# Optimization experiments

Measured on AMD Instinct MI355X. Metric: run time of the kernel, lower is better.

The kernel has to match this reference:

```python
import jax, jax.numpy as jnp
import numpy as np

N = 100000   # nodes
E = 1600000  # edges
C = 128      # in_channels
H = 128      # hidden_channels


def _gcn_conv(x, row, col, w, W, b, n_nodes):
    """PyG-style GCNConv: x' = D^{-1/2}(A+I)D^{-1/2} (x W) + b, with edge weights."""
    x = x @ W  # [N, out]
    # add self-loops with weight 1
    loop = jnp.arange(n_nodes, dtype=row.dtype)
    row2 = jnp.concatenate([row, loop])
    col2 = jnp.concatenate([col, loop])
    w2 = jnp.concatenate([w, jnp.ones((n_nodes,), dtype=w.dtype)])
    # symmetric normalization: deg over destination (col), per PyG gcn_norm
    deg = jax.ops.segment_sum(w2, col2, num_segments=n_nodes)
    dinv = jnp.where(deg > 0, jax.lax.rsqrt(jnp.where(deg > 0, deg, 1.0)), 0.0)
    norm = dinv[row2] * w2 * dinv[col2]  # [E+N]
    # message = norm * x[src]; aggregate (scatter-add) into dst
    msg = norm[:, None] * x[row2]  # [E+N, out]
    out = jax.ops.segment_sum(msg, col2, num_segments=n_nodes)
    return out + b


def setup_inputs() -> dict:
    key = jax.random.key(0)
    k0, k1, k2, k3, k4 = jax.random.split(key, 5)
    node_feature = jax.random.normal(k0, (N, C), dtype=jnp.float32)
    edge_index = jax.random.randint(k1, (2, E), 0, N, dtype=jnp.int32)
    edge_weight = jax.random.uniform(k2, (E,), dtype=jnp.float32)
    W1 = jax.random.normal(k3, (C, H), dtype=jnp.float32) * (1.0 / np.sqrt(C))
    b1 = jnp.zeros((H,), dtype=jnp.float32)
    W2 = jax.random.normal(k4, (H, 1), dtype=jnp.float32) * (1.0 / np.sqrt(H))
    b2 = jnp.zeros((1,), dtype=jnp.float32)
    return {"node_feature": node_feature, "edge_index": edge_index,
            "edge_weight": edge_weight, "W1": W1, "b1": b1, "W2": W2, "b2": b2}


def reference(node_feature, edge_index, edge_weight, W1, b1, W2, b2):
    row, col = edge_index[0], edge_index[1]
    h = _gcn_conv(node_feature, row, col, edge_weight, W1, b1, N)
    out = _gcn_conv(h, row, col, edge_weight, W2, b2, N)  # [N, 1]
    return out
```

## Files before the change

### kernel.cpp

```cpp
#include <hip/hip_runtime.h>

#define CH 128
#define CHUNK 8192
#define BSH 9
#define BNODES 512
#define MAXB 256

__global__ __launch_bounds__(256) void k_uw(const float* __restrict__ W1,
                                            const float* __restrict__ b1,
                                            const float* __restrict__ W2,
                                            float* __restrict__ u) {
    int wid  = blockIdx.x * 4 + (threadIdx.x >> 6);
    if (wid > CH) return;
    int lane = threadIdx.x & 63;
    const float* rowp = (wid < CH) ? (W1 + (size_t)wid * CH) : b1;
    float2 xv = *(const float2*)(rowp + lane * 2);
    float2 vv = *(const float2*)(W2 + lane * 2);
    float acc = xv.x * vv.x + xv.y * vv.y;
#pragma unroll
    for (int m = 32; m; m >>= 1) acc += __shfl_xor(acc, m);
    if (lane == 0) u[wid] = acc;
}

__global__ __launch_bounds__(256) void k_gemv(const float* __restrict__ X,
                                              const float* __restrict__ v,
                                              float* __restrict__ t, int n) {
    int wv   = blockIdx.x * 4 + (threadIdx.x >> 6);
    int lane = threadIdx.x & 63;
    int row  = wv * 2 + (lane >> 5);
    if (row >= n) return;
    float4 xv = *(const float4*)(X + (size_t)row * CH + (lane & 31) * 4);
    float4 vv = *(const float4*)(v + (lane & 31) * 4);
    float acc = xv.x * vv.x + xv.y * vv.y + xv.z * vv.z + xv.w * vv.w;
#pragma unroll
    for (int m = 16; m; m >>= 1) acc += __shfl_xor(acc, m);
    if ((lane & 31) == 0) t[row] = acc;
}

__global__ __launch_bounds__(256) void k_hist(const int* __restrict__ col,
                                              int* __restrict__ Ht,
                                              int nbuck, int e_cnt) {
    __shared__ int h[MAXB];
    int b = blockIdx.x, tid = threadIdx.x;
    if (tid < nbuck) h[tid] = 0;
    __syncthreads();
    int e0 = b * CHUNK, e1 = min(e0 + CHUNK, e_cnt);
    for (int e = e0 + tid; e < e1; e += 256)
        atomicAdd(&h[col[e] >> BSH], 1);
    __syncthreads();
    if (tid < nbuck) Ht[(size_t)b * nbuck + tid] = h[tid];
}

__global__ __launch_bounds__(256) void k_colscan(const int* __restrict__ Ht,
                                                 int* __restrict__ Hs,
                                                 int* __restrict__ coltot,
                                                 int nchunk, int nbuck) {
    int j = blockIdx.x * 4 + (threadIdx.x >> 6);
    if (j >= nbuck) return;
    int lane = threadIdx.x & 63;
    int run = 0;
    for (int base = 0; base < nchunk; base += 64) {
        int idx = base + lane;
        int v = (idx < nchunk) ? Ht[(size_t)idx * nbuck + j] : 0;
        int incl = v;
#pragma unroll
        for (int d = 1; d < 64; d <<= 1) {
            int up = __shfl_up(incl, d);
            if (lane >= d) incl += up;
        }
        if (idx < nchunk) Hs[(size_t)idx * nbuck + j] = run + incl - v;
        run += __shfl(incl, 63);
    }
    if (lane == 0) coltot[j] = run;
}

__global__ __launch_bounds__(256) void k_permute(const int* __restrict__ row,
                                                 const int* __restrict__ col,
                                                 const float* __restrict__ w,
                                                 const int* __restrict__ Hs,
                                                 const int* __restrict__ coltot,
                                                 int* __restrict__ bstart,
                                                 int2* __restrict__ ep,
                                                 int nbuck, int e_cnt) {
    __shared__ int ct[MAXB];
    __shared__ int bs[MAXB + 1];
    __shared__ int cur[MAXB];
    int b = blockIdx.x, tid = threadIdx.x;
    for (int k = tid; k < nbuck; k += 256) ct[k] = coltot[k];
    __syncthreads();
    if (tid < 64) {
        int vals[4]; int sum = 0;
#pragma unroll
        for (int k = 0; k < 4; ++k) {
            int idx = tid * 4 + k;
            vals[k] = (idx < nbuck) ? ct[idx] : 0;
            sum += vals[k];
        }
        int incl = sum;
#pragma unroll
        for (int d = 1; d < 64; d <<= 1) {
            int up = __shfl_up(incl, d);
            if (tid >= d) incl += up;
        }
        int run = incl - sum;
#pragma unroll
        for (int k = 0; k < 4; ++k) {
            int idx = tid * 4 + k;
            if (idx < nbuck) bs[idx] = run;
            run += vals[k];
        }
        if (tid == 63) bs[nbuck] = run;
    }
    __syncthreads();
    for (int k = tid; k < nbuck; k += 256) cur[k] = bs[k] + Hs[(size_t)b * nbuck + k];
    __syncthreads();
    int e0 = b * CHUNK, e1 = min(e0 + CHUNK, e_cnt);
    for (int e = e0 + tid; e < e1; e += 256) {
        int r = row[e], c = col[e];
        float wv = w[e];
        int pos = atomicAdd(&cur[c >> BSH], 1);
        ep[pos] = make_int2(r | ((c & (BNODES - 1)) << 17), __float_as_int(wv));
    }
    if (b == 0)
        for (int k = tid; k <= nbuck; k += 256) bstart[k] = bs[k];
}

__global__ __launch_bounds__(512) void k_adeg(const int2* __restrict__ ep,
                                              const int* __restrict__ bstart,
                                              const float* __restrict__ t,
                                              float* __restrict__ dinv,
                                              float* __restrict__ p, int n) {
    __shared__ float acc[BNODES];
    int b = blockIdx.x, tid = threadIdx.x;
    acc[tid] = 0.f;
    __syncthreads();
    int j1 = bstart[b + 1];
    for (int j = bstart[b] + tid; j < j1; j += 512) {
        int2 kv = ep[j];
        atomicAdd(&acc[kv.x >> 17], __int_as_float(kv.y));
    }
    __syncthreads();
    int node = (b << BSH) + tid;
    if (node < n) {
        float di = rsqrtf(1.0f + acc[tid]);
        dinv[node] = di;
        p[node] = di * t[node];
    }
}

__global__ __launch_bounds__(512) void k_as1(const int2* __restrict__ ep,
                                             const int* __restrict__ bstart,
                                             const float* __restrict__ p,
                                             const float* __restrict__ dinv,
                                             const float* __restrict__ u,
                                             float* __restrict__ q, int n) {
    __shared__ float acc[BNODES];
    int b = blockIdx.x, tid = threadIdx.x;
    acc[tid] = 0.f;
    __syncthreads();
    int j1 = bstart[b + 1];
    for (int j = bstart[b] + tid; j < j1; j += 512) {
        int2 kv = ep[j];
        atomicAdd(&acc[kv.x >> 17], __int_as_float(kv.y) * p[kv.x & 0x1FFFF]);
    }
    __syncthreads();
    int node = (b << BSH) + tid;
    if (node < n) {
        float di = dinv[node];
        float s1 = di * (p[node] + acc[tid]);
        q[node] = di * (s1 + u[CH]);
    }
}

__global__ __launch_bounds__(512) void k_aout(const int2* __restrict__ ep,
                                              const int* __restrict__ bstart,
                                              const float* __restrict__ q,
                                              const float* __restrict__ dinv,
                                              const float* __restrict__ b2,
                                              float* __restrict__ out, int n) {
    __shared__ float acc[BNODES];
    int b = blockIdx.x, tid = threadIdx.x;
    acc[tid] = 0.f;
    __syncthreads();
    int j1 = bstart[b + 1];
    for (int j = bstart[b] + tid; j < j1; j += 512) {
        int2 kv = ep[j];
        atomicAdd(&acc[kv.x >> 17], __int_as_float(kv.y) * q[kv.x & 0x1FFFF]);
    }
    __syncthreads();
    int node = (b << BSH) + tid;
    if (node < n)
        out[node] = b2[0] + dinv[node] * (q[node] + acc[tid]);
}

extern "C" void kernel_launch(void* const* d_in, const int* in_sizes, int n_in,
                              void* d_out, int out_size, void* d_ws, size_t ws_size,
                              hipStream_t stream) {
    const float* x   = (const float*)d_in[0];
    const int*   ei  = (const int*)d_in[1];
    const float* w   = (const float*)d_in[2];
    const float* W1  = (const float*)d_in[3];
    const float* b1  = (const float*)d_in[4];
    const float* W2  = (const float*)d_in[5];
    const float* b2  = (const float*)d_in[6];
    float* out = (float*)d_out;

    const int n     = in_sizes[0] / CH;
    const int e_cnt = in_sizes[2];
    const int* row = ei;
    const int* col = ei + e_cnt;

    const int nbuck  = (n + BNODES - 1) >> BSH;
    const int nchunk = (e_cnt + CHUNK - 1) / CHUNK;

    int2*  ep     = (int2*)d_ws;
    float* u      = (float*)(ep + e_cnt);
    float* t      = u + 132;
    float* dinv   = t + n;
    float* p      = dinv + n;
    float* q      = p + n;
    int*   coltot = (int*)(q + n);
    int*   bstart = coltot + nbuck;
    int*   Ht     = bstart + nbuck + 1;
    int*   Hs     = Ht + (size_t)nchunk * nbuck;

    k_uw<<<(CH + 1 + 3) / 4, 256, 0, stream>>>(W1, b1, W2, u);
    k_gemv<<<(n + 7) / 8, 256, 0, stream>>>(x, u, t, n);

    k_hist<<<nchunk, 256, 0, stream>>>(col, Ht, nbuck, e_cnt);
    k_colscan<<<(nbuck + 3) / 4, 256, 0, stream>>>(Ht, Hs, coltot, nchunk, nbuck);
    k_permute<<<nchunk, 256, 0, stream>>>(row, col, w, Hs, coltot, bstart, ep, nbuck, e_cnt);

    k_adeg<<<nbuck, 512, 0, stream>>>(ep, bstart, t, dinv, p, n);
    k_as1<<<nbuck, 512, 0, stream>>>(ep, bstart, p, dinv, u, q, n);
    k_aout<<<nbuck, 512, 0, stream>>>(ep, bstart, q, dinv, b2, out, n);
}
```

Measured before the change: 174.3 us.

## Fuse sort and aggregation stages into one persistent kernel with grid barriers

Replaces the six separate histogram, scan, permute and three aggregation kernels with a single kernel that synchronises stages through a software grid barrier built on global atomics. The column scan is folded into each block, which re-reads the histogram table. The GEMV is also turned into a grid-stride loop over four rows per iteration with a fixed grid. The aim is to remove launch overhead and the gaps between dependent kernels. In exchange it relies on all blocks (about 196) being co-resident to avoid deadlock, and adds a redundant O(nchunk) scan per block plus barrier spin cost.

```diff
diff --git a/kernel.cpp b/kernel.cpp
--- a/kernel.cpp
+++ b/kernel.cpp
@@ -5,11 +5,32 @@
 #define BSH 9
 #define BNODES 512
 #define MAXB 256
+#define NT 512
+
+__device__ __forceinline__ void gsync(int* bar, int nb, int it) {
+    __syncthreads();
+    if (threadIdx.x == 0) {
+        __threadfence();
+        if (__hip_atomic_fetch_add(&bar[0], 1, __ATOMIC_ACQ_REL,
+                                   __HIP_MEMORY_SCOPE_AGENT) == nb - 1) {
+            __hip_atomic_store(&bar[0], 0, __ATOMIC_RELAXED, __HIP_MEMORY_SCOPE_AGENT);
+            __hip_atomic_fetch_add(&bar[1], 1, __ATOMIC_RELEASE, __HIP_MEMORY_SCOPE_AGENT);
+        } else {
+            while (__hip_atomic_load(&bar[1], __ATOMIC_ACQUIRE,
+                                     __HIP_MEMORY_SCOPE_AGENT) < it)
+                __builtin_amdgcn_s_sleep(8);
+        }
+        __threadfence();
+    }
+    __syncthreads();
+}
 
 __global__ __launch_bounds__(256) void k_uw(const float* __restrict__ W1,
                                             const float* __restrict__ b1,
                                             const float* __restrict__ W2,
-                                            float* __restrict__ u) {
+                                            float* __restrict__ u,
+                                            int* __restrict__ bar) {
+    if (blockIdx.x == 0 && threadIdx.x == 0) { bar[0] = 0; bar[1] = 0; }
     int wid  = blockIdx.x * 4 + (threadIdx.x >> 6);
     if (wid > CH) return;
     int lane = threadIdx.x & 63;
@@ -23,174 +44,172 @@
 }
 
 __global__ __launch_bounds__(256) void k_gemv(const float* __restrict__ X,
-                                              const float* __restrict__ v,
+                                              const float* __restrict__ u,
                                               float* __restrict__ t, int n) {
-    int wv   = blockIdx.x * 4 + (threadIdx.x >> 6);
-    int lane = threadIdx.x & 63;
-    int row  = wv * 2 + (lane >> 5);
-    if (row >= n) return;
-    float4 xv = *(const float4*)(X + (size_t)row * CH + (lane & 31) * 4);
-    float4 vv = *(const float4*)(v + (lane & 31) * 4);
-    float acc = xv.x * vv.x + xv.y * vv.y + xv.z * vv.z + xv.w * vv.w;
-#pragma unroll
-    for (int m = 16; m; m >>= 1) acc += __shfl_xor(acc, m);
-    if ((lane & 31) == 0) t[row] = acc;
-}
-
-__global__ __launch_bounds__(256) void k_hist(const int* __restrict__ col,
-                                              int* __restrict__ Ht,
-                                              int nbuck, int e_cnt) {
-    __shared__ int h[MAXB];
-    int b = blockIdx.x, tid = threadIdx.x;
-    if (tid < nbuck) h[tid] = 0;
-    __syncthreads();
-    int e0 = b * CHUNK, e1 = min(e0 + CHUNK, e_cnt);
-    for (int e = e0 + tid; e < e1; e += 256)
-        atomicAdd(&h[col[e] >> BSH], 1);
-    __syncthreads();
-    if (tid < nbuck) Ht[(size_t)b * nbuck + tid] = h[tid];
-}
-
-__global__ __launch_bounds__(256) void k_colscan(const int* __restrict__ Ht,
-                                                 int* __restrict__ Hs,
-                                                 int* __restrict__ coltot,
-                                                 int nchunk, int nbuck) {
-    int j = blockIdx.x * 4 + (threadIdx.x >> 6);
-    if (j >= nbuck) return;
-    int lane = threadIdx.x & 63;
-    int run = 0;
-    for (int base = 0; base < nchunk; base += 64) {
-        int idx = base + lane;
-        int v = (idx < nchunk) ? Ht[(size_t)idx * nbuck + j] : 0;
-        int incl = v;
-#pragma unroll
-        for (int d = 1; d < 64; d <<= 1) {
-            int up = __shfl_up(incl, d);
-            if (lane >= d) incl += up;
-        }
-        if (idx < nchunk) Hs[(size_t)idx * nbuck + j] = run + incl - v;
-        run += __shfl(incl, 63);
-    }
-    if (lane == 0) coltot[j] = run;
-}
-
-__global__ __launch_bounds__(256) void k_permute(const int* __restrict__ row,
-                                                 const int* __restrict__ col,
-                                                 const float* __restrict__ w,
-                                                 const int* __restrict__ Hs,
-                                                 const int* __restrict__ coltot,
-                                                 int* __restrict__ bstart,
-                                                 int2* __restrict__ ep,
-                                                 int nbuck, int e_cnt) {
-    __shared__ int ct[MAXB];
-    __shared__ int bs[MAXB + 1];
-    __shared__ int cur[MAXB];
-    int b = blockIdx.x, tid = threadIdx.x;
-    for (int k = tid; k < nbuck; k += 256) ct[k] = coltot[k];
-    __syncthreads();
-    if (tid < 64) {
-        int vals[4]; int sum = 0;
-#pragma unroll
-        for (int k = 0; k < 4; ++k) {
-            int idx = tid * 4 + k;
-            vals[k] = (idx < nbuck) ? ct[idx] : 0;
-            sum += vals[k];
-        }
-        int incl = sum;
-#pragma unroll
-        for (int d = 1; d < 64; d <<= 1) {
-            int up = __shfl_up(incl, d);
-            if (tid >= d) incl += up;
-        }
-        int run = incl - sum;
-#pragma unroll
-        for (int k = 0; k < 4; ++k) {
-            int idx = tid * 4 + k;
-            if (idx < nbuck) bs[idx] = run;
-            run += vals[k];
-        }
-        if (tid == 63) bs[nbuck] = run;
-    }
-    __syncthreads();
-    for (int k = tid; k < nbuck; k += 256) cur[k] = bs[k] + Hs[(size_t)b * nbuck + k];
-    __syncthreads();
-    int e0 = b * CHUNK, e1 = min(e0 + CHUNK, e_cnt);
-    for (int e = e0 + tid; e < e1; e += 256) {
-        int r = row[e], c = col[e];
-        float wv = w[e];
-        int pos = atomicAdd(&cur[c >> BSH], 1);
-        ep[pos] = make_int2(r | ((c & (BNODES - 1)) << 17), __float_as_int(wv));
-    }
-    if (b == 0)
-        for (int k = tid; k <= nbuck; k += 256) bstart[k] = bs[k];
-}
-
-__global__ __launch_bounds__(512) void k_adeg(const int2* __restrict__ ep,
-                                              const int* __restrict__ bstart,
-                                              const float* __restrict__ t,
-                                              float* __restrict__ dinv,
-                                              float* __restrict__ p, int n) {
-    __shared__ float acc[BNODES];
-    int b = blockIdx.x, tid = threadIdx.x;
-    acc[tid] = 0.f;
-    __syncthreads();
-    int j1 = bstart[b + 1];
-    for (int j = bstart[b] + tid; j < j1; j += 512) {
-        int2 kv = ep[j];
-        atomicAdd(&acc[kv.x >> 17], __int_as_float(kv.y));
-    }
-    __syncthreads();
-    int node = (b << BSH) + tid;
-    if (node < n) {
-        float di = rsqrtf(1.0f + acc[tid]);
-        dinv[node] = di;
-        p[node] = di * t[node];
-    }
-}
-
-__global__ __launch_bounds__(512) void k_as1(const int2* __restrict__ ep,
-                                             const int* __restrict__ bstart,
-                                             const float* __restrict__ p,
-                                             const float* __restrict__ dinv,
+    int hw = blockIdx.x * 8 + (threadIdx.x >> 5);
+    int l  = threadIdx.x & 31;
+    float4 uv = *(const float4*)(u + l * 4);
+    const int stride = gridDim.x * 8;
+    for (int base = hw; base < n; base += stride * 4) {
+        int r0 = base, r1 = base + stride, r2 = base + 2 * stride, r3 = base + 3 * stride;
+        float a0 = 0.f, a1 = 0.f, a2 = 0.f, a3 = 0.f;
+        if (r0 < n) { float4 x = *(const float4*)(X + (size_t)r0 * CH + l * 4);
+                      a0 = x.x * uv.x + x.y * uv.y + x.z * uv.z + x.w * uv.w; }
+        if (r1 < n) { float4 x = *(const float4*)(X + (size_t)r1 * CH + l * 4);
+                      a1 = x.x * uv.x + x.y * uv.y + x.z * uv.z + x.w * uv.w; }
+        if (r2 < n) { float4 x = *(const float4*)(X + (size_t)r2 * CH + l * 4);
+                      a2 = x.x * uv.x + x.y * uv.y + x.z * uv.z + x.w * uv.w; }
+        if (r3 < n) { float4 x = *(const float4*)(X + (size_t)r3 * CH + l * 4);
+                      a3 = x.x * uv.x + x.y * uv.y + x.z * uv.z + x.w * uv.w; }
+#pragma unroll
+        for (int m = 16; m; m >>= 1) {
+            a0 += __shfl_xor(a0, m); a1 += __shfl_xor(a1, m);
+            a2 += __shfl_xor(a2, m); a3 += __shfl_xor(a3, m);
+        }
+        if (l == 0) {
+            if (r0 < n) t[r0] = a0;
+            if (r1 < n) t[r1] = a1;
+            if (r2 < n) t[r2] = a2;
+            if (r3 < n) t[r3] = a3;
+        }
+    }
+}
+
+__global__ __launch_bounds__(NT) void k_mega(const int* __restrict__ row,
+                                             const int* __restrict__ col,
+                                             const float* __restrict__ w,
+                                             const float* __restrict__ t,
                                              const float* __restrict__ u,
-                                             float* __restrict__ q, int n) {
-    __shared__ float acc[BNODES];
-    int b = blockIdx.x, tid = threadIdx.x;
-    acc[tid] = 0.f;
-    __syncthreads();
-    int j1 = bstart[b + 1];
-    for (int j = bstart[b] + tid; j < j1; j += 512) {
-        int2 kv = ep[j];
-        atomicAdd(&acc[kv.x >> 17], __int_as_float(kv.y) * p[kv.x & 0x1FFFF]);
-    }
-    __syncthreads();
-    int node = (b << BSH) + tid;
-    if (node < n) {
-        float di = dinv[node];
-        float s1 = di * (p[node] + acc[tid]);
-        q[node] = di * (s1 + u[CH]);
-    }
-}
-
-__global__ __launch_bounds__(512) void k_aout(const int2* __restrict__ ep,
-                                              const int* __restrict__ bstart,
-                                              const float* __restrict__ q,
-                                              const float* __restrict__ dinv,
-                                              const float* __restrict__ b2,
-                                              float* __restrict__ out, int n) {
-    __shared__ float acc[BNODES];
-    int b = blockIdx.x, tid = threadIdx.x;
-    acc[tid] = 0.f;
-    __syncthreads();
-    int j1 = bstart[b + 1];
-    for (int j = bstart[b] + tid; j < j1; j += 512) {
-        int2 kv = ep[j];
-        atomicAdd(&acc[kv.x >> 17], __int_as_float(kv.y) * q[kv.x & 0x1FFFF]);
-    }
-    __syncthreads();
-    int node = (b << BSH) + tid;
-    if (node < n)
-        out[node] = b2[0] + dinv[node] * (q[node] + acc[tid]);
+                                             const float* __restrict__ b2,
+                                             int2* __restrict__ ep,
+                                             int* __restrict__ Ht,
+                                             int* __restrict__ bstart,
+                                             int* __restrict__ bar,
+                                             float* __restrict__ dinv,
+                                             float* __restrict__ p,
+                                             float* __restrict__ q,
+                                             float* __restrict__ out,
+                                             int n, int e_cnt, int nbuck, int nchunk) {
+    __shared__ int smem[3 * MAXB + 4];
+    int*   h    = smem;
+    int*   runS = smem;
+    int*   curS = smem + MAXB;
+    int*   bs   = smem + 2 * MAXB;
+    float* acc  = (float*)smem;
+
+    const int b = blockIdx.x, tid = threadIdx.x;
+    const int nb = gridDim.x;
+
+    if (b < nchunk) {
+        if (tid < nbuck) h[tid] = 0;
+        __syncthreads();
+        int e0 = b * CHUNK, e1 = min(e0 + CHUNK, e_cnt);
+        for (int e = e0 + tid; e < e1; e += NT)
+            atomicAdd(&h[col[e] >> BSH], 1);
+        __syncthreads();
+        if (tid < nbuck) Ht[(size_t)b * nbuck + tid] = h[tid];
+    }
+    gsync(bar, nb, 1);
+
+    if (b < nchunk) {
+        if (tid < nbuck) {
+            int run = 0, pre = 0;
+            for (int c = 0; c < nchunk; ++c) {
+                int v = Ht[(size_t)c * nbuck + tid];
+                run += v;
+                if (c < b) pre += v;
+            }
+            runS[tid] = run;
+            curS[tid] = pre;
+        }
+        __syncthreads();
+        if (tid < 64) {
+            int vals[4]; int sum = 0;
+#pragma unroll
+            for (int k = 0; k < 4; ++k) {
+                int idx = tid * 4 + k;
+                vals[k] = (idx < nbuck) ? runS[idx] : 0;
+                sum += vals[k];
+            }
+            int incl = sum;
+#pragma unroll
+            for (int d = 1; d < 64; d <<= 1) {
+                int up = __shfl_up(incl, d);
+                if (tid >= d) incl += up;
+            }
+            int run2 = incl - sum;
+#pragma unroll
+            for (int k = 0; k < 4; ++k) {
+                int idx = tid * 4 + k;
+                if (idx < nbuck) bs[idx] = run2;
+                run2 += vals[k];
+            }
+            if (tid == 63) bs[nbuck] = run2;
+        }
+        __syncthreads();
+        if (tid < nbuck) curS[tid] += bs[tid];
+        __syncthreads();
+        int e0 = b * CHUNK, e1 = min(e0 + CHUNK, e_cnt);
+        for (int e = e0 + tid; e < e1; e += NT) {
+            int r = row[e], c = col[e];
+            float wv = w[e];
+            int pos = atomicAdd(&curS[c >> BSH], 1);
+            ep[pos] = make_int2(r | ((c & (BNODES - 1)) << 17), __float_as_int(wv));
+        }
+        if (b == 0 && tid <= nbuck) bstart[tid] = bs[tid];
+    }
+    gsync(bar, nb, 2);
+
+    if (b < nbuck) {
+        acc[tid] = 0.f;
+        __syncthreads();
+        int j0 = bstart[b], j1 = bstart[b + 1];
+        for (int j = j0 + tid; j < j1; j += NT) {
+            int2 kv = ep[j];
+            atomicAdd(&acc[kv.x >> 17], __int_as_float(kv.y));
+        }
+        __syncthreads();
+        int node = (b << BSH) + tid;
+        if (node < n) {
+            float di = rsqrtf(1.0f + acc[tid]);
+            dinv[node] = di;
+            p[node] = di * t[node];
+        }
+    }
+    gsync(bar, nb, 3);
+
+    if (b < nbuck) {
+        acc[tid] = 0.f;
+        __syncthreads();
+        float beta = u[CH];
+        int j0 = bstart[b], j1 = bstart[b + 1];
+        for (int j = j0 + tid; j < j1; j += NT) {
+            int2 kv = ep[j];
+            atomicAdd(&acc[kv.x >> 17], __int_as_float(kv.y) * p[kv.x & 0x1FFFF]);
+        }
+        __syncthreads();
+        int node = (b << BSH) + tid;
+        if (node < n) {
+            float di = dinv[node];
+            float s1 = di * (p[node] + acc[tid]);
+            q[node] = di * (s1 + beta);
+        }
+    }
+    gsync(bar, nb, 4);
+
+    if (b < nbuck) {
+        acc[tid] = 0.f;
+        __syncthreads();
+        int j0 = bstart[b], j1 = bstart[b + 1];
+        for (int j = j0 + tid; j < j1; j += NT) {
+            int2 kv = ep[j];
+            atomicAdd(&acc[kv.x >> 17], __int_as_float(kv.y) * q[kv.x & 0x1FFFF]);
+        }
+        __syncthreads();
+        int node = (b << BSH) + tid;
+        if (node < n)
+            out[node] = b2[0] + dinv[node] * (q[node] + acc[tid]);
+    }
 }
 
 extern "C" void kernel_launch(void* const* d_in, const int* in_sizes, int n_in,
@@ -212,6 +231,7 @@
 
     const int nbuck  = (n + BNODES - 1) >> BSH;
     const int nchunk = (e_cnt + CHUNK - 1) / CHUNK;
+    const int nblk   = (nbuck > nchunk) ? nbuck : nchunk;
 
     int2*  ep     = (int2*)d_ws;
     float* u      = (float*)(ep + e_cnt);
@@ -219,19 +239,14 @@
     float* dinv   = t + n;
     float* p      = dinv + n;
     float* q      = p + n;
-    int*   coltot = (int*)(q + n);
-    int*   bstart = coltot + nbuck;
-    int*   Ht     = bstart + nbuck + 1;
-    int*   Hs     = Ht + (size_t)nchunk * nbuck;
-
-    k_uw<<<(CH + 1 + 3) / 4, 256, 0, stream>>>(W1, b1, W2, u);
-    k_gemv<<<(n + 7) / 8, 256, 0, stream>>>(x, u, t, n);
-
-    k_hist<<<nchunk, 256, 0, stream>>>(col, Ht, nbuck, e_cnt);
-    k_colscan<<<(nbuck + 3) / 4, 256, 0, stream>>>(Ht, Hs, coltot, nchunk, nbuck);
-    k_permute<<<nchunk, 256, 0, stream>>>(row, col, w, Hs, coltot, bstart, ep, nbuck, e_cnt);
-
-    k_adeg<<<nbuck, 512, 0, stream>>>(ep, bstart, t, dinv, p, n);
-    k_as1<<<nbuck, 512, 0, stream>>>(ep, bstart, p, dinv, u, q, n);
-    k_aout<<<nbuck, 512, 0, stream>>>(ep, bstart, q, dinv, b2, out, n);
-}
+    int*   bstart = (int*)(q + n);
+    int*   bar    = bstart + nbuck + 1;
+    int*   Ht     = bar + 2;
+
+    k_uw<<<(CH + 1 + 3) / 4, 256, 0, stream>>>(W1, b1, W2, u, bar);
+    k_gemv<<<1024, 256, 0, stream>>>(x, u, t, n);
+    k_mega<<<nblk, NT, 0, stream>>>(row, col, w, t, u, b2,
+                                    ep, Ht, bstart, bar,
+                                    dinv, p, q, out,
+                                    n, e_cnt, nbuck, nchunk);
+}
```

New measurement: 311.3 us. 78.6% more time.

## Fuse small kernels horizontally and shrink buckets to raise aggregation parallelism

Applied to the files above, without the earlier changes.

Merges the W1·W2 projection into the histogram kernel and the column scan into a grid-stride GEMV kernel. This cuts the launch count from eight to six and lets independent work share a grid. Bucket size drops from 512 to 256 nodes, giving about twice as many aggregation blocks, which now run 1024 threads each, and the permute kernel moves to 512 threads with a wave-serial bucket-offset scan. The GEMV now handles four rows per half-wave per iteration for more memory-level parallelism. In exchange, smaller buckets make the histogram and scan matrices larger, and 1024-thread blocks may reduce occupancy flexibility.

```diff
diff --git a/kernel.cpp b/kernel.cpp
--- a/kernel.cpp
+++ b/kernel.cpp
@@ -2,79 +2,104 @@
 
 #define CH 128
 #define CHUNK 8192
-#define BSH 9
-#define BNODES 512
-#define MAXB 256
-
-__global__ __launch_bounds__(256) void k_uw(const float* __restrict__ W1,
-                                            const float* __restrict__ b1,
-                                            const float* __restrict__ W2,
-                                            float* __restrict__ u) {
-    int wid  = blockIdx.x * 4 + (threadIdx.x >> 6);
-    if (wid > CH) return;
-    int lane = threadIdx.x & 63;
-    const float* rowp = (wid < CH) ? (W1 + (size_t)wid * CH) : b1;
-    float2 xv = *(const float2*)(rowp + lane * 2);
-    float2 vv = *(const float2*)(W2 + lane * 2);
-    float acc = xv.x * vv.x + xv.y * vv.y;
-#pragma unroll
-    for (int m = 32; m; m >>= 1) acc += __shfl_xor(acc, m);
-    if (lane == 0) u[wid] = acc;
-}
-
-__global__ __launch_bounds__(256) void k_gemv(const float* __restrict__ X,
-                                              const float* __restrict__ v,
-                                              float* __restrict__ t, int n) {
-    int wv   = blockIdx.x * 4 + (threadIdx.x >> 6);
-    int lane = threadIdx.x & 63;
-    int row  = wv * 2 + (lane >> 5);
-    if (row >= n) return;
-    float4 xv = *(const float4*)(X + (size_t)row * CH + (lane & 31) * 4);
-    float4 vv = *(const float4*)(v + (lane & 31) * 4);
-    float acc = xv.x * vv.x + xv.y * vv.y + xv.z * vv.z + xv.w * vv.w;
-#pragma unroll
-    for (int m = 16; m; m >>= 1) acc += __shfl_xor(acc, m);
-    if ((lane & 31) == 0) t[row] = acc;
-}
-
-__global__ __launch_bounds__(256) void k_hist(const int* __restrict__ col,
-                                              int* __restrict__ Ht,
-                                              int nbuck, int e_cnt) {
+#define BSH 8
+#define BNODES 256
+#define MAXB 512
+#define PNT 512
+#define AGG_NT 1024
+#define GEMV_BLOCKS 1024
+
+__global__ __launch_bounds__(256) void k_uw_hist(const float* __restrict__ W1,
+                                                 const float* __restrict__ b1,
+                                                 const float* __restrict__ W2,
+                                                 float* __restrict__ u,
+                                                 const int* __restrict__ col,
+                                                 int* __restrict__ Ht,
+                                                 int nbuck, int nchunk, int e_cnt) {
     __shared__ int h[MAXB];
     int b = blockIdx.x, tid = threadIdx.x;
-    if (tid < nbuck) h[tid] = 0;
+    if (b == nchunk) {
+        int wv = tid >> 6, lane = tid & 63;
+        float2 vv = *(const float2*)(W2 + lane * 2);
+        for (int r = wv; r <= CH; r += 4) {
+            const float* rowp = (r < CH) ? (W1 + (size_t)r * CH) : b1;
+            float2 xv = *(const float2*)(rowp + lane * 2);
+            float acc = xv.x * vv.x + xv.y * vv.y;
+#pragma unroll
+            for (int m = 32; m; m >>= 1) acc += __shfl_xor(acc, m);
+            if (lane == 0) u[r] = acc;
+        }
+        return;
+    }
+    for (int k = tid; k < nbuck; k += 256) h[k] = 0;
     __syncthreads();
     int e0 = b * CHUNK, e1 = min(e0 + CHUNK, e_cnt);
     for (int e = e0 + tid; e < e1; e += 256)
         atomicAdd(&h[col[e] >> BSH], 1);
     __syncthreads();
-    if (tid < nbuck) Ht[(size_t)b * nbuck + tid] = h[tid];
-}
-
-__global__ __launch_bounds__(256) void k_colscan(const int* __restrict__ Ht,
-                                                 int* __restrict__ Hs,
-                                                 int* __restrict__ coltot,
-                                                 int nchunk, int nbuck) {
-    int j = blockIdx.x * 4 + (threadIdx.x >> 6);
-    if (j >= nbuck) return;
-    int lane = threadIdx.x & 63;
-    int run = 0;
-    for (int base = 0; base < nchunk; base += 64) {
-        int idx = base + lane;
-        int v = (idx < nchunk) ? Ht[(size_t)idx * nbuck + j] : 0;
-        int incl = v;
-#pragma unroll
-        for (int d = 1; d < 64; d <<= 1) {
-            int up = __shfl_up(incl, d);
-            if (lane >= d) incl += up;
-        }
-        if (idx < nchunk) Hs[(size_t)idx * nbuck + j] = run + incl - v;
-        run += __shfl(incl, 63);
-    }
-    if (lane == 0) coltot[j] = run;
-}
-
-__global__ __launch_bounds__(256) void k_permute(const int* __restrict__ row,
+    for (int k = tid; k < nbuck; k += 256) Ht[(size_t)b * nbuck + k] = h[k];
+}
+
+__global__ __launch_bounds__(256) void k_gemv_colscan(const float* __restrict__ X,
+                                                      const float* __restrict__ u,
+                                                      float* __restrict__ t,
+                                                      const int* __restrict__ Ht,
+                                                      int* __restrict__ Hs,
+                                                      int* __restrict__ coltot,
+                                                      int n, int nchunk, int nbuck,
+                                                      int nbCols) {
+    int b = blockIdx.x, tid = threadIdx.x;
+    if (b < nbCols) {
+        int j = b * 4 + (tid >> 6);
+        if (j >= nbuck) return;
+        int lane = tid & 63;
+        int run = 0;
+        for (int base = 0; base < nchunk; base += 64) {
+            int idx = base + lane;
+            int v = (idx < nchunk) ? Ht[(size_t)idx * nbuck + j] : 0;
+            int incl = v;
+#pragma unroll
+            for (int d = 1; d < 64; d <<= 1) {
+                int up = __shfl_up(incl, d);
+                if (lane >= d) incl += up;
+            }
+            if (idx < nchunk) Hs[(size_t)idx * nbuck + j] = run + incl - v;
+            run += __shfl(incl, 63);
+        }
+        if (lane == 0) coltot[j] = run;
+        return;
+    }
+    int gb = b - nbCols;
+    int hw = gb * 8 + (tid >> 5);
+    int l  = tid & 31;
+    float4 uv = *(const float4*)(u + l * 4);
+    const int stride = GEMV_BLOCKS * 8;
+    for (int base = hw; base < n; base += stride * 4) {
+        int r0 = base, r1 = base + stride, r2 = base + 2 * stride, r3 = base + 3 * stride;
+        float a0 = 0.f, a1 = 0.f, a2 = 0.f, a3 = 0.f;
+        if (r0 < n) { float4 x = *(const float4*)(X + (size_t)r0 * CH + l * 4);
+                      a0 = x.x * uv.x + x.y * uv.y + x.z * uv.z + x.w * uv.w; }
+        if (r1 < n) { float4 x = *(const float4*)(X + (size_t)r1 * CH + l * 4);
+                      a1 = x.x * uv.x + x.y * uv.y + x.z * uv.z + x.w * uv.w; }
+        if (r2 < n) { float4 x = *(const float4*)(X + (size_t)r2 * CH + l * 4);
+                      a2 = x.x * uv.x + x.y * uv.y + x.z * uv.z + x.w * uv.w; }
+        if (r3 < n) { float4 x = *(const float4*)(X + (size_t)r3 * CH + l * 4);
+                      a3 = x.x * uv.x + x.y * uv.y + x.z * uv.z + x.w * uv.w; }
+#pragma unroll
+        for (int m = 16; m; m >>= 1) {
+            a0 += __shfl_xor(a0, m); a1 += __shfl_xor(a1, m);
+            a2 += __shfl_xor(a2, m); a3 += __shfl_xor(a3, m);
+        }
+        if (l == 0) {
+            if (r0 < n) t[r0] = a0;
+            if (r1 < n) t[r1] = a1;
+            if (r2 < n) t[r2] = a2;
+            if (r3 < n) t[r3] = a3;
+        }
+    }
+}
+
+__global__ __launch_bounds__(PNT) void k_permute(const int* __restrict__ row,
                                                  const int* __restrict__ col,
                                                  const float* __restrict__ w,
                                                  const int* __restrict__ Hs,
@@ -82,114 +107,105 @@
                                                  int* __restrict__ bstart,
                                                  int2* __restrict__ ep,
                                                  int nbuck, int e_cnt) {
-    __shared__ int ct[MAXB];
     __shared__ int bs[MAXB + 1];
     __shared__ int cur[MAXB];
     int b = blockIdx.x, tid = threadIdx.x;
-    for (int k = tid; k < nbuck; k += 256) ct[k] = coltot[k];
-    __syncthreads();
     if (tid < 64) {
-        int vals[4]; int sum = 0;
-#pragma unroll
-        for (int k = 0; k < 4; ++k) {
-            int idx = tid * 4 + k;
-            vals[k] = (idx < nbuck) ? ct[idx] : 0;
-            sum += vals[k];
-        }
-        int incl = sum;
-#pragma unroll
-        for (int d = 1; d < 64; d <<= 1) {
-            int up = __shfl_up(incl, d);
-            if (tid >= d) incl += up;
-        }
-        int run = incl - sum;
-#pragma unroll
-        for (int k = 0; k < 4; ++k) {
-            int idx = tid * 4 + k;
-            if (idx < nbuck) bs[idx] = run;
-            run += vals[k];
-        }
-        if (tid == 63) bs[nbuck] = run;
-    }
-    __syncthreads();
-    for (int k = tid; k < nbuck; k += 256) cur[k] = bs[k] + Hs[(size_t)b * nbuck + k];
+        int run = 0;
+        for (int base = 0; base < nbuck; base += 64) {
+            int idx = base + tid;
+            int v = (idx < nbuck) ? coltot[idx] : 0;
+            int incl = v;
+#pragma unroll
+            for (int d = 1; d < 64; d <<= 1) {
+                int up = __shfl_up(incl, d);
+                if (tid >= d) incl += up;
+            }
+            if (idx < nbuck) bs[idx] = run + incl - v;
+            run += __shfl(incl, 63);
+        }
+        if (tid == 0) bs[nbuck] = run;
+    }
+    __syncthreads();
+    for (int k = tid; k < nbuck; k += PNT)
+        cur[k] = bs[k] + Hs[(size_t)b * nbuck + k];
     __syncthreads();
     int e0 = b * CHUNK, e1 = min(e0 + CHUNK, e_cnt);
-    for (int e = e0 + tid; e < e1; e += 256) {
+    for (int e = e0 + tid; e < e1; e += PNT) {
         int r = row[e], c = col[e];
         float wv = w[e];
         int pos = atomicAdd(&cur[c >> BSH], 1);
         ep[pos] = make_int2(r | ((c & (BNODES - 1)) << 17), __float_as_int(wv));
     }
     if (b == 0)
-        for (int k = tid; k <= nbuck; k += 256) bstart[k] = bs[k];
-}
-
-__global__ __launch_bounds__(512) void k_adeg(const int2* __restrict__ ep,
-                                              const int* __restrict__ bstart,
-                                              const float* __restrict__ t,
-                                              float* __restrict__ dinv,
-                                              float* __restrict__ p, int n) {
+        for (int k = tid; k <= nbuck; k += PNT) bstart[k] = bs[k];
+}
+
+__global__ __launch_bounds__(AGG_NT) void k_adeg(const int2* __restrict__ ep,
+                                                 const int* __restrict__ bstart,
+                                                 const float* __restrict__ t,
+                                                 float* __restrict__ dinv,
+                                                 float* __restrict__ p, int n) {
     __shared__ float acc[BNODES];
     int b = blockIdx.x, tid = threadIdx.x;
-    acc[tid] = 0.f;
+    if (tid < BNODES) acc[tid] = 0.f;
     __syncthreads();
     int j1 = bstart[b + 1];
-    for (int j = bstart[b] + tid; j < j1; j += 512) {
+    for (int j = bstart[b] + tid; j < j1; j += AGG_NT) {
         int2 kv = ep[j];
         atomicAdd(&acc[kv.x >> 17], __int_as_float(kv.y));
     }
     __syncthreads();
     int node = (b << BSH) + tid;
-    if (node < n) {
+    if (tid < BNODES && node < n) {
         float di = rsqrtf(1.0f + acc[tid]);
         dinv[node] = di;
         p[node] = di * t[node];
     }
 }
 
-__global__ __launch_bounds__(512) void k_as1(const int2* __restrict__ ep,
-                                             const int* __restrict__ bstart,
-                                             const float* __restrict__ p,
-                                             const float* __restrict__ dinv,
-                                             const float* __restrict__ u,
-                                             float* __restrict__ q, int n) {
+__global__ __launch_bounds__(AGG_NT) void k_as1(const int2* __restrict__ ep,
+                                                const int* __restrict__ bstart,
+                                                const float* __restrict__ p,
+                                                const float* __restrict__ dinv,
+                                                const float* __restrict__ u,
+                                                float* __restrict__ q, int n) {
     __shared__ float acc[BNODES];
     int b = blockIdx.x, tid = threadIdx.x;
-    acc[tid] = 0.f;
+    if (tid < BNODES) acc[tid] = 0.f;
     __syncthreads();
     int j1 = bstart[b + 1];
-    for (int j = bstart[b] + tid; j < j1; j += 512) {
+    for (int j = bstart[b] + tid; j < j1; j += AGG_NT) {
         int2 kv = ep[j];
         atomicAdd(&acc[kv.x >> 17], __int_as_float(kv.y) * p[kv.x & 0x1FFFF]);
     }
     __syncthreads();
     int node = (b << BSH) + tid;
-    if (node < n) {
+    if (tid < BNODES && node < n) {
         float di = dinv[node];
         float s1 = di * (p[node] + acc[tid]);
         q[node] = di * (s1 + u[CH]);
     }
 }
 
-__global__ __launch_bounds__(512) void k_aout(const int2* __restrict__ ep,
-                                              const int* __restrict__ bstart,
-                                              const float* __restrict__ q,
-                                              const float* __restrict__ dinv,
-                                              const float* __restrict__ b2,
-                                              float* __restrict__ out, int n) {
+__global__ __launch_bounds__(AGG_NT) void k_aout(const int2* __restrict__ ep,
+                                                 const int* __restrict__ bstart,
+                                                 const float* __restrict__ q,
+                                                 const float* __restrict__ dinv,
+                                                 const float* __restrict__ b2,
+                                                 float* __restrict__ out, int n) {
     __shared__ float acc[BNODES];
     int b = blockIdx.x, tid = threadIdx.x;
-    acc[tid] = 0.f;
+    if (tid < BNODES) acc[tid] = 0.f;
     __syncthreads();
     int j1 = bstart[b + 1];
-    for (int j = bstart[b] + tid; j < j1; j += 512) {
+    for (int j = bstart[b] + tid; j < j1; j += AGG_NT) {
         int2 kv = ep[j];
         atomicAdd(&acc[kv.x >> 17], __int_as_float(kv.y) * q[kv.x & 0x1FFFF]);
     }
     __syncthreads();
     int node = (b << BSH) + tid;
-    if (node < n)
+    if (tid < BNODES && node < n)
         out[node] = b2[0] + dinv[node] * (q[node] + acc[tid]);
 }
 
@@ -212,6 +228,7 @@
 
     const int nbuck  = (n + BNODES - 1) >> BSH;
     const int nchunk = (e_cnt + CHUNK - 1) / CHUNK;
+    const int nbCols = (nbuck + 3) / 4;
 
     int2*  ep     = (int2*)d_ws;
     float* u      = (float*)(ep + e_cnt);
@@ -224,14 +241,13 @@
     int*   Ht     = bstart + nbuck + 1;
     int*   Hs     = Ht + (size_t)nchunk * nbuck;
 
-    k_uw<<<(CH + 1 + 3) / 4, 256, 0, stream>>>(W1, b1, W2, u);
-    k_gemv<<<(n + 7) / 8, 256, 0, stream>>>(x, u, t, n);
-
-    k_hist<<<nchunk, 256, 0, stream>>>(col, Ht, nbuck, e_cnt);
-    k_colscan<<<(nbuck + 3) / 4, 256, 0, stream>>>(Ht, Hs, coltot, nchunk, nbuck);
-    k_permute<<<nchunk, 256, 0, stream>>>(row, col, w, Hs, coltot, bstart, ep, nbuck, e_cnt);
-
-    k_adeg<<<nbuck, 512, 0, stream>>>(ep, bstart, t, dinv, p, n);
-    k_as1<<<nbuck, 512, 0, stream>>>(ep, bstart, p, dinv, u, q, n);
-    k_aout<<<nbuck, 512, 0, stream>>>(ep, bstart, q, dinv, b2, out, n);
-}
+    k_uw_hist<<<nchunk + 1, 256, 0, stream>>>(W1, b1, W2, u, col, Ht,
+                                              nbuck, nchunk, e_cnt);
+    k_gemv_colscan<<<nbCols + GEMV_BLOCKS, 256, 0, stream>>>(x, u, t, Ht, Hs, coltot,
+                                                             n, nchunk, nbuck, nbCols);
+    k_permute<<<nchunk, PNT, 0, stream>>>(row, col, w, Hs, coltot, bstart, ep,
+                                          nbuck, e_cnt);
+    k_adeg<<<nbuck, AGG_NT, 0, stream>>>(ep, bstart, t, dinv, p, n);
+    k_as1<<<nbuck, AGG_NT, 0, stream>>>(ep, bstart, p, dinv, u, q, n);
+    k_aout<<<nbuck, AGG_NT, 0, stream>>>(ep, bstart, q, dinv, b2, out, n);
+}
```

Result: slower. 181.3 us (+4.0%).
